# Optimization experiments

Measured on AMD Instinct MI355X. Metric: run time of the kernel, lower is better.

Reference implementation:

```python
import jax, jax.numpy as jnp
import numpy as np

N_NODES = 50000
N_EDGES = 600000
D_OBJ = 128
D_REL = 128
D_OUT = 128


def setup_inputs() -> dict:
    key = jax.random.key(0)
    ks = jax.random.split(key, 7)
    s_obj = 1.0 / np.sqrt(D_OBJ)
    s_rel = 1.0 / np.sqrt(D_REL)
    return {
        "obj_vecs": jax.random.normal(ks[0], (N_NODES, D_OBJ), dtype=jnp.float32),
        "rel_vecs": jax.random.normal(ks[1], (N_EDGES, D_REL), dtype=jnp.float32),
        "edge_index": jax.random.randint(ks[2], (N_EDGES, 2), 0, N_NODES, dtype=jnp.int64),
        "W_obj": jax.random.normal(ks[3], (D_OUT, D_OBJ), dtype=jnp.float32) * s_obj,
        "b_obj": jax.random.normal(ks[4], (D_OUT,), dtype=jnp.float32) * s_obj,
        "W_rel": jax.random.normal(ks[5], (D_OUT, D_REL), dtype=jnp.float32) * s_rel,
        "b_rel": jax.random.normal(ks[6], (D_OUT,), dtype=jnp.float32) * s_rel,
    }


def reference(obj_vecs, rel_vecs, edge_index, W_obj, b_obj, W_rel, b_rel):
    # Per-node linear once ([N, d_out]) instead of twice per edge -- same math
    # since lin_obj(x_i) + lin_obj(x_j) = (x_i W^T + b) + (x_j W^T + b).
    obj_lin = obj_vecs @ W_obj.T + b_obj            # [N, d_out]
    rel_lin = rel_vecs @ W_rel.T + b_rel            # [E, d_out]
    src = edge_index[:, 0]
    dst = edge_index[:, 1]
    # message = relu(lin_obj(obj_i) + lin_rel(rel_k) + lin_obj(obj_j))
    msg = jax.nn.relu(obj_lin[src] + rel_lin + obj_lin[dst])  # [E, d_out]
    # aggr='add', flow source_to_target: scatter-add at target nodes (col 1)
    aggr = jax.ops.segment_sum(msg, dst, num_segments=obj_vecs.shape[0])
    return jax.nn.relu(aggr)
```

## Files before the change

kernel.cpp:

```cpp
#include <hip/hip_runtime.h>

#define N_NODES 50000
#define N_EDGES 600000
#define DD 128

typedef __attribute__((ext_vector_type(8))) short short8;
typedef __attribute__((ext_vector_type(4))) float f32x4;

__device__ __forceinline__ short f2bf(float f) {
    union { float f; unsigned u; } v; v.f = f;
    unsigned r = v.u + 0x7fffu + ((v.u >> 16) & 1u);
    return (short)(r >> 16);
}
__device__ __forceinline__ float bf2f(short s) {
    union { float f; unsigned u; } v; v.u = ((unsigned)(unsigned short)s) << 16;
    return v.f;
}
__device__ __forceinline__ float u2f(unsigned u) {
    union { float f; unsigned u; } v; v.u = u;
    return v.f;
}
__device__ __forceinline__ unsigned packbf(float a, float b) {
    return ((unsigned)(unsigned short)f2bf(a)) |
           (((unsigned)(unsigned short)f2bf(b)) << 16);
}

__global__ __launch_bounds__(256) void k_lin(const float* __restrict__ X,
                                             const float* __restrict__ W,
                                             const float* __restrict__ bias,
                                             short* __restrict__ Y,
                                             int ntiles) {
    __shared__ __align__(16) short Wf[128 * 128];
    for (int i = threadIdx.x; i < 2048; i += 256) {
        const int fl = i & 63, fr = i >> 6;
        const int nt = fr >> 2, ks = fr & 3, fg = fl >> 4, fln = fl & 15;
        const float* s = W + (nt * 16 + fln) * DD + ks * 32 + fg * 8;
        short* d = Wf + i * 8;
#pragma unroll
        for (int j = 0; j < 8; ++j) d[j] = f2bf(s[j]);
    }
    __syncthreads();

    const int wave = threadIdx.x >> 6;
    const int lane = threadIdx.x & 63;
    const int g = lane >> 4, ln = lane & 15;

    float bb[8];
#pragma unroll
    for (int nt = 0; nt < 8; ++nt) bb[nt] = bias[nt * 16 + ln];

    for (int t = blockIdx.x * 4 + wave; t < ntiles; t += gridDim.x * 4) {
        const float* xr = X + (size_t)(t * 16 + ln) * DD;
        short8 a[4];
#pragma unroll
        for (int ks = 0; ks < 4; ++ks) {
            const f32x4* p = (const f32x4*)(xr + ks * 32 + g * 8);
            const f32x4 t0 = __builtin_nontemporal_load(p);
            const f32x4 t1 = __builtin_nontemporal_load(p + 1);
            short8 v;
            v[0] = f2bf(t0[0]); v[1] = f2bf(t0[1]); v[2] = f2bf(t0[2]); v[3] = f2bf(t0[3]);
            v[4] = f2bf(t1[0]); v[5] = f2bf(t1[1]); v[6] = f2bf(t1[2]); v[7] = f2bf(t1[3]);
            a[ks] = v;
        }
#pragma unroll
        for (int nt = 0; nt < 8; ++nt) {
            f32x4 acc = {0.f, 0.f, 0.f, 0.f};
#pragma unroll
            for (int ks = 0; ks < 4; ++ks) {
                short8 b = *(const short8*)(Wf + (((nt << 2) + ks) * 64 + lane) * 8);
                acc = __builtin_amdgcn_mfma_f32_16x16x32_bf16(a[ks], b, acc, 0, 0, 0);
            }
#pragma unroll
            for (int r = 0; r < 4; ++r)
                Y[(size_t)(t * 16 + g * 4 + r) * DD + nt * 16 + ln] = f2bf(acc[r] + bb[nt]);
        }
    }
}

__global__ __launch_bounds__(256) void k_count(const int* __restrict__ EI,
                                               int* __restrict__ counts) {
    int e = blockIdx.x * 256 + threadIdx.x;
    if (e < N_EDGES) atomicAdd(&counts[EI[2 * e + 1]], 1);
}

__global__ __launch_bounds__(256) void k_scan1(const int* __restrict__ counts,
                                               int* __restrict__ scanned,
                                               int* __restrict__ bsum) {
    __shared__ int tmp[256];
    const int t = threadIdx.x;
    const int i = blockIdx.x * 256 + t;
    int v = (i < N_NODES) ? counts[i] : 0;
    tmp[t] = v;
    __syncthreads();
#pragma unroll
    for (int off = 1; off < 256; off <<= 1) {
        int x = (t >= off) ? tmp[t - off] : 0;
        __syncthreads();
        tmp[t] += x;
        __syncthreads();
    }
    if (i < N_NODES) scanned[i] = tmp[t] - v;
    if (t == 255) bsum[blockIdx.x] = tmp[255];
}

__global__ __launch_bounds__(256) void k_scan3m(const int* __restrict__ scanned,
                                                const int* __restrict__ bsum,
                                                int* __restrict__ offsets,
                                                int* __restrict__ cursor,
                                                int nb) {
    __shared__ int red[256];
    const int t = threadIdx.x;
    const int bid = blockIdx.x;
    red[t] = (t < bid && t < nb) ? bsum[t] : 0;
    __syncthreads();
#pragma unroll
    for (int off = 128; off > 0; off >>= 1) {
        if (t < off) red[t] += red[t + off];
        __syncthreads();
    }
    const int pre = red[0];
    const int i = bid * 256 + t;
    if (i < N_NODES) {
        const int off = scanned[i] + pre;
        offsets[i] = off;
        cursor[i] = off;
    }
    if (i == 0) offsets[N_NODES] = N_EDGES;
}

__global__ __launch_bounds__(256) void k_scatter2(const int* __restrict__ EI,
                                                  int* __restrict__ cursor,
                                                  int* __restrict__ perm) {
    int e = blockIdx.x * 256 + threadIdx.x;
    if (e < N_EDGES)
        perm[e] = atomicAdd(&cursor[EI[2 * e + 1]], 1);
}

__global__ __launch_bounds__(256) void k_fl(const float* __restrict__ RV,
                                            const int* __restrict__ EI,
                                            const int* __restrict__ perm,
                                            const float* __restrict__ W,
                                            const float* __restrict__ bias,
                                            const short* __restrict__ OL,
                                            unsigned* __restrict__ Ysw) {
    __shared__ __align__(16) short Wf[128 * 128];
    __shared__ __align__(16) unsigned stg[4][8 * 136];

    for (int i = threadIdx.x; i < 2048; i += 256) {
        const int fl = i & 63, fr = i >> 6;
        const int nt = fr >> 2, ks = fr & 3, fg = fl >> 4, fln = fl & 15;
        const float* s = W + (nt * 16 + fln) * DD + ks * 32 + fg * 8;
        short* d = Wf + i * 8;
#pragma unroll
        for (int j = 0; j < 8; ++j) d[j] = f2bf(s[j]);
    }
    __syncthreads();

    const int wave = threadIdx.x >> 6;
    const int lane = threadIdx.x & 63;
    const int g = lane >> 4, ln = lane & 15;
    unsigned* st = stg[wave];

    const float br0 = bias[2 * lane];
    const float br1 = bias[2 * lane + 1];
    const unsigned short* OLu = (const unsigned short*)OL;
    const int NT = N_EDGES / 16;

    for (int t = blockIdx.x * 4 + wave; t < NT; t += gridDim.x * 4) {
        const int e0 = t * 16;

        const float* xr = RV + (size_t)(e0 + ln) * DD;
        short8 a[4];
#pragma unroll
        for (int ks = 0; ks < 4; ++ks) {
            const f32x4* p = (const f32x4*)(xr + ks * 32 + g * 8);
            const f32x4 t0 = __builtin_nontemporal_load(p);
            const f32x4 t1 = __builtin_nontemporal_load(p + 1);
            short8 v;
            v[0] = f2bf(t0[0]); v[1] = f2bf(t0[1]); v[2] = f2bf(t0[2]); v[3] = f2bf(t0[3]);
            v[4] = f2bf(t1[0]); v[5] = f2bf(t1[1]); v[6] = f2bf(t1[2]); v[7] = f2bf(t1[3]);
            a[ks] = v;
        }

        int sp = 0, pp = 0;
        if (lane < 16) {
            sp = EI[2 * (e0 + lane)];
            pp = perm[e0 + lane];
        }

        f32x4 acc[8];
#pragma unroll
        for (int nt = 0; nt < 8; ++nt) {
            acc[nt] = (f32x4){0.f, 0.f, 0.f, 0.f};
#pragma unroll
            for (int ks = 0; ks < 4; ++ks) {
                short8 b = *(const short8*)(Wf + (((nt << 2) + ks) * 64 + lane) * 8);
                acc[nt] = __builtin_amdgcn_mfma_f32_16x16x32_bf16(a[ks], b, acc[nt], 0, 0, 0);
            }
        }

#pragma unroll
        for (int nt = 0; nt < 8; ++nt) {
            const int c = nt * 16 + ln;
            st[(g * 2) * 136 + c]     = packbf(acc[nt][0], acc[nt][1]);
            st[(g * 2 + 1) * 136 + c] = packbf(acc[nt][2], acc[nt][3]);
        }

#pragma unroll
        for (int ep = 0; ep < 8; ++ep) {
            const unsigned qx = st[ep * 136 + 2 * lane];
            const unsigned qy = st[ep * 136 + 2 * lane + 1];
#pragma unroll
            for (int sub = 0; sub < 2; ++sub) {
                const int e = 2 * ep + sub;
                const int src = __shfl(sp, e);
                const int pos = __shfl(pp, e);
                const float s0 = sub ? u2f(qx & 0xffff0000u) : u2f(qx << 16);
                const float s1 = sub ? u2f(qy & 0xffff0000u) : u2f(qy << 16);
                const unsigned olw = *(const unsigned*)(OLu + (size_t)src * DD + 2 * lane);
                const float y0 = s0 + br0 + u2f(olw << 16);
                const float y1 = s1 + br1 + u2f(olw & 0xffff0000u);
                Ysw[(size_t)pos * (DD / 2) + lane] = packbf(y0, y1);
            }
        }
    }
}

__global__ __launch_bounds__(256) void k_segsum(const unsigned* __restrict__ Ysw,
                                                const short* __restrict__ OL,
                                                const int* __restrict__ offs,
                                                float* __restrict__ out) {
    const int wave = threadIdx.x >> 6;
    const int lane = threadIdx.x & 63;
    const int v = blockIdx.x * 4 + wave;
    if (v >= N_NODES) return;

    const int r0 = offs[v], r1 = offs[v + 1];
    const int half = lane >> 5;
    const int q = lane & 31;
    const unsigned short* OLu = (const unsigned short*)OL;

    const uint2 odw = *(const uint2*)(OLu + (size_t)v * DD + 4 * q);
    const float od0 = u2f(odw.x << 16), od1 = u2f(odw.x & 0xffff0000u);
    const float od2 = u2f(odw.y << 16), od3 = u2f(odw.y & 0xffff0000u);

    float a0 = 0.f, a1 = 0.f, a2 = 0.f, a3 = 0.f;
    for (int r = r0 + half; r < r1; r += 2) {
        const uint2 y = *(const uint2*)(Ysw + (size_t)r * (DD / 2) + 2 * q);
        a0 += fmaxf(u2f(y.x << 16) + od0, 0.f);
        a1 += fmaxf(u2f(y.x & 0xffff0000u) + od1, 0.f);
        a2 += fmaxf(u2f(y.y << 16) + od2, 0.f);
        a3 += fmaxf(u2f(y.y & 0xffff0000u) + od3, 0.f);
    }
    a0 += __shfl_xor(a0, 32);
    a1 += __shfl_xor(a1, 32);
    a2 += __shfl_xor(a2, 32);
    a3 += __shfl_xor(a3, 32);

    if (half == 0) {
        float4 o;
        o.x = fmaxf(a0, 0.f); o.y = fmaxf(a1, 0.f);
        o.z = fmaxf(a2, 0.f); o.w = fmaxf(a3, 0.f);
        *(float4*)(out + (size_t)v * DD + 4 * q) = o;
    }
}

extern "C" void kernel_launch(void* const* d_in, const int* in_sizes, int n_in,
                              void* d_out, int out_size, void* d_ws, size_t ws_size,
                              hipStream_t stream) {
    const float* obj = (const float*)d_in[0];
    const float* rel = (const float*)d_in[1];
    const int*   ei  = (const int*)d_in[2];
    const float* Wo  = (const float*)d_in[3];
    const float* bo  = (const float*)d_in[4];
    const float* Wr  = (const float*)d_in[5];
    const float* br  = (const float*)d_in[6];
    float* out = (float*)d_out;

    char* ws = (char*)d_ws;
    unsigned* Ysw  = (unsigned*)ws;
    short* OLb     = (short*)(ws + 153600000);
    int*   perm    = (int*)(ws + 166400000);
    int*   counts  = (int*)(ws + 168800000);
    int*   scanned = (int*)(ws + 169000192);
    int*   offsets = (int*)(ws + 169200896);
    int*   cursor  = (int*)(ws + 169401600);
    int*   bsum    = (int*)(ws + 169601792);

    const int NB_E = (N_EDGES + 255) / 256;
    const int NB_N = (N_NODES + 255) / 256;

    hipMemsetAsync(counts, 0, N_NODES * sizeof(int), stream);
    k_count<<<NB_E, 256, 0, stream>>>(ei, counts);
    k_scan1<<<NB_N, 256, 0, stream>>>(counts, scanned, bsum);
    k_scan3m<<<NB_N, 256, 0, stream>>>(scanned, bsum, offsets, cursor, NB_N);
    k_scatter2<<<NB_E, 256, 0, stream>>>(ei, cursor, perm);
    k_lin<<<782, 256, 0, stream>>>(obj, Wo, bo, OLb, N_NODES / 16);
    k_fl<<<2048, 256, 0, stream>>>(rel, ei, perm, Wr, br, OLb, Ysw);
    k_segsum<<<(N_NODES + 3) / 4, 256, 0, stream>>>(Ysw, OLb, offsets, out);
}
```

Baseline: 238.2 us.

## Fuse edge linear with segmented aggregation over destination-sorted edges

Instead of writing a bf16 per-edge message buffer in permuted order and reducing it in a separate segment-sum kernel, edges are sorted by destination (storing edge id and source) and each wave processes a fixed run of 80 sorted edges. It gathers rel rows, runs the MFMA linear, and accumulates relu messages directly into the output, using atomics only for segments shared across run boundaries. This removes the large intermediate buffer write and read, at the cost of gathered (non-contiguous) rel_vecs loads, an extra zero-fill and relu pass, and float atomics. The second gather of obj_lin[dst] per edge is now done inside the fused kernel.

```diff
diff --git a/kernel.cpp b/kernel.cpp
--- a/kernel.cpp
+++ b/kernel.cpp
@@ -3,6 +3,8 @@
 #define N_NODES 50000
 #define N_EDGES 600000
 #define DD 128
+#define RUNE 80
+#define NBLK_AGG 1875
 
 typedef __attribute__((ext_vector_type(8))) short short8;
 typedef __attribute__((ext_vector_type(4))) float f32x4;
@@ -11,10 +13,6 @@
     union { float f; unsigned u; } v; v.f = f;
     unsigned r = v.u + 0x7fffu + ((v.u >> 16) & 1u);
     return (short)(r >> 16);
-}
-__device__ __forceinline__ float bf2f(short s) {
-    union { float f; unsigned u; } v; v.u = ((unsigned)(unsigned short)s) << 16;
-    return v.f;
 }
 __device__ __forceinline__ float u2f(unsigned u) {
     union { float f; unsigned u; } v; v.u = u;
@@ -54,9 +52,8 @@
         short8 a[4];
 #pragma unroll
         for (int ks = 0; ks < 4; ++ks) {
-            const f32x4* p = (const f32x4*)(xr + ks * 32 + g * 8);
-            const f32x4 t0 = __builtin_nontemporal_load(p);
-            const f32x4 t1 = __builtin_nontemporal_load(p + 1);
+            const f32x4 t0 = *(const f32x4*)(xr + ks * 32 + g * 8);
+            const f32x4 t1 = *(const f32x4*)(xr + ks * 32 + g * 8 + 4);
             short8 v;
             v[0] = f2bf(t0[0]); v[1] = f2bf(t0[1]); v[2] = f2bf(t0[2]); v[3] = f2bf(t0[3]);
             v[4] = f2bf(t1[0]); v[5] = f2bf(t1[1]); v[6] = f2bf(t1[2]); v[7] = f2bf(t1[3]);
@@ -105,7 +102,6 @@
 
 __global__ __launch_bounds__(256) void k_scan3m(const int* __restrict__ scanned,
                                                 const int* __restrict__ bsum,
-                                                int* __restrict__ offsets,
                                                 int* __restrict__ cursor,
                                                 int nb) {
     __shared__ int red[256];
@@ -120,29 +116,29 @@
     }
     const int pre = red[0];
     const int i = bid * 256 + t;
-    if (i < N_NODES) {
-        const int off = scanned[i] + pre;
-        offsets[i] = off;
-        cursor[i] = off;
-    }
-    if (i == 0) offsets[N_NODES] = N_EDGES;
-}
-
-__global__ __launch_bounds__(256) void k_scatter2(const int* __restrict__ EI,
+    if (i < N_NODES) cursor[i] = scanned[i] + pre;
+}
+
+__global__ __launch_bounds__(256) void k_scatter3(const int* __restrict__ EI,
                                                   int* __restrict__ cursor,
-                                                  int* __restrict__ perm) {
+                                                  int2* __restrict__ sorted,
+                                                  int* __restrict__ dsts) {
     int e = blockIdx.x * 256 + threadIdx.x;
-    if (e < N_EDGES)
-        perm[e] = atomicAdd(&cursor[EI[2 * e + 1]], 1);
-}
-
-__global__ __launch_bounds__(256) void k_fl(const float* __restrict__ RV,
-                                            const int* __restrict__ EI,
-                                            const int* __restrict__ perm,
-                                            const float* __restrict__ W,
-                                            const float* __restrict__ bias,
-                                            const short* __restrict__ OL,
-                                            unsigned* __restrict__ Ysw) {
+    if (e < N_EDGES) {
+        int2 sd = *(const int2*)(EI + 2 * e);
+        int pos = atomicAdd(&cursor[sd.y], 1);
+        sorted[pos] = make_int2(e, sd.x);
+        dsts[pos] = sd.y;
+    }
+}
+
+__global__ __launch_bounds__(256) void k_fagg2(const float* __restrict__ RV,
+                                               const int2* __restrict__ sorted,
+                                               const int* __restrict__ dsts,
+                                               const float* __restrict__ W,
+                                               const float* __restrict__ bias,
+                                               const short* __restrict__ OL,
+                                               float* __restrict__ out) {
     __shared__ __align__(16) short Wf[128 * 128];
     __shared__ __align__(16) unsigned stg[4][8 * 136];
 
@@ -161,33 +157,58 @@
     const int g = lane >> 4, ln = lane & 15;
     unsigned* st = stg[wave];
 
+    const int wid = blockIdx.x * 4 + wave;
+    const int p0 = wid * RUNE;
+    const int p1 = p0 + RUNE;
+
     const float br0 = bias[2 * lane];
     const float br1 = bias[2 * lane + 1];
     const unsigned short* OLu = (const unsigned short*)OL;
-    const int NT = N_EDGES / 16;
-
-    for (int t = blockIdx.x * 4 + wave; t < NT; t += gridDim.x * 4) {
-        const int e0 = t * 16;
-
-        const float* xr = RV + (size_t)(e0 + ln) * DD;
-        short8 a[4];
+
+    const bool head_shared = (p0 > 0) && (dsts[p0 - 1] == dsts[p0]);
+    const bool tail_shared = (p1 < N_EDGES) && (dsts[p1] == dsts[p1 - 1]);
+
+    int d_cur = dsts[p0];
+    bool head_atomic = head_shared;
+    float a0 = 0.f, a1 = 0.f;
+
+    int2 se_c = sorted[p0 + ln];
+    int  dl_c = dsts[p0 + ln];
+    f32x4 ar_c[8];
+    {
+        const float* base = RV + (size_t)se_c.x * DD;
 #pragma unroll
         for (int ks = 0; ks < 4; ++ks) {
-            const f32x4* p = (const f32x4*)(xr + ks * 32 + g * 8);
-            const f32x4 t0 = __builtin_nontemporal_load(p);
-            const f32x4 t1 = __builtin_nontemporal_load(p + 1);
+            ar_c[2 * ks]     = *(const f32x4*)(base + ks * 32 + g * 8);
+            ar_c[2 * ks + 1] = *(const f32x4*)(base + ks * 32 + g * 8 + 4);
+        }
+    }
+
+    for (int k = 0; k < RUNE / 16; ++k) {
+        int2 se_n = se_c; int dl_n = dl_c;
+        f32x4 ar_n[8];
+        const bool have = (k + 1) < (RUNE / 16);
+        if (have) {
+            const int e0n = p0 + (k + 1) * 16;
+            se_n = sorted[e0n + ln];
+            dl_n = dsts[e0n + ln];
+            const float* base = RV + (size_t)se_n.x * DD;
+#pragma unroll
+            for (int ks = 0; ks < 4; ++ks) {
+                ar_n[2 * ks]     = *(const f32x4*)(base + ks * 32 + g * 8);
+                ar_n[2 * ks + 1] = *(const f32x4*)(base + ks * 32 + g * 8 + 4);
+            }
+        }
+
+        short8 af[4];
+#pragma unroll
+        for (int ks = 0; ks < 4; ++ks) {
+            const f32x4 t0 = ar_c[2 * ks], t1 = ar_c[2 * ks + 1];
             short8 v;
             v[0] = f2bf(t0[0]); v[1] = f2bf(t0[1]); v[2] = f2bf(t0[2]); v[3] = f2bf(t0[3]);
             v[4] = f2bf(t1[0]); v[5] = f2bf(t1[1]); v[6] = f2bf(t1[2]); v[7] = f2bf(t1[3]);
-            a[ks] = v;
-        }
-
-        int sp = 0, pp = 0;
-        if (lane < 16) {
-            sp = EI[2 * (e0 + lane)];
-            pp = perm[e0 + lane];
-        }
-
+            af[ks] = v;
+        }
         f32x4 acc[8];
 #pragma unroll
         for (int nt = 0; nt < 8; ++nt) {
@@ -195,7 +216,7 @@
 #pragma unroll
             for (int ks = 0; ks < 4; ++ks) {
                 short8 b = *(const short8*)(Wf + (((nt << 2) + ks) * 64 + lane) * 8);
-                acc[nt] = __builtin_amdgcn_mfma_f32_16x16x32_bf16(a[ks], b, acc[nt], 0, 0, 0);
+                acc[nt] = __builtin_amdgcn_mfma_f32_16x16x32_bf16(af[ks], b, acc[nt], 0, 0, 0);
             }
         }
 
@@ -213,55 +234,58 @@
 #pragma unroll
             for (int sub = 0; sub < 2; ++sub) {
                 const int e = 2 * ep + sub;
-                const int src = __shfl(sp, e);
-                const int pos = __shfl(pp, e);
+                const int src  = __shfl(se_c.y, e);
+                const int dstv = __shfl(dl_c, e);
+                if (dstv != d_cur) {
+                    if (head_atomic) {
+                        atomicAdd(&out[(size_t)d_cur * DD + 2 * lane], a0);
+                        atomicAdd(&out[(size_t)d_cur * DD + 2 * lane + 1], a1);
+                        head_atomic = false;
+                    } else {
+                        *(float2*)(out + (size_t)d_cur * DD + 2 * lane) =
+                            make_float2(a0, a1);
+                    }
+                    a0 = a1 = 0.f;
+                    d_cur = dstv;
+                }
                 const float s0 = sub ? u2f(qx & 0xffff0000u) : u2f(qx << 16);
                 const float s1 = sub ? u2f(qy & 0xffff0000u) : u2f(qy << 16);
-                const unsigned olw = *(const unsigned*)(OLu + (size_t)src * DD + 2 * lane);
-                const float y0 = s0 + br0 + u2f(olw << 16);
-                const float y1 = s1 + br1 + u2f(olw & 0xffff0000u);
-                Ysw[(size_t)pos * (DD / 2) + lane] = packbf(y0, y1);
+                const unsigned ows = *(const unsigned*)(OLu + (size_t)src  * DD + 2 * lane);
+                const unsigned owd = *(const unsigned*)(OLu + (size_t)dstv * DD + 2 * lane);
+                const float m0 = s0 + br0 + u2f(ows << 16) + u2f(owd << 16);
+                const float m1 = s1 + br1 + u2f(ows & 0xffff0000u) + u2f(owd & 0xffff0000u);
+                a0 += fmaxf(m0, 0.f);
+                a1 += fmaxf(m1, 0.f);
             }
         }
-    }
-}
-
-__global__ __launch_bounds__(256) void k_segsum(const unsigned* __restrict__ Ysw,
-                                                const short* __restrict__ OL,
-                                                const int* __restrict__ offs,
-                                                float* __restrict__ out) {
-    const int wave = threadIdx.x >> 6;
-    const int lane = threadIdx.x & 63;
-    const int v = blockIdx.x * 4 + wave;
-    if (v >= N_NODES) return;
-
-    const int r0 = offs[v], r1 = offs[v + 1];
-    const int half = lane >> 5;
-    const int q = lane & 31;
-    const unsigned short* OLu = (const unsigned short*)OL;
-
-    const uint2 odw = *(const uint2*)(OLu + (size_t)v * DD + 4 * q);
-    const float od0 = u2f(odw.x << 16), od1 = u2f(odw.x & 0xffff0000u);
-    const float od2 = u2f(odw.y << 16), od3 = u2f(odw.y & 0xffff0000u);
-
-    float a0 = 0.f, a1 = 0.f, a2 = 0.f, a3 = 0.f;
-    for (int r = r0 + half; r < r1; r += 2) {
-        const uint2 y = *(const uint2*)(Ysw + (size_t)r * (DD / 2) + 2 * q);
-        a0 += fmaxf(u2f(y.x << 16) + od0, 0.f);
-        a1 += fmaxf(u2f(y.x & 0xffff0000u) + od1, 0.f);
-        a2 += fmaxf(u2f(y.y << 16) + od2, 0.f);
-        a3 += fmaxf(u2f(y.y & 0xffff0000u) + od3, 0.f);
-    }
-    a0 += __shfl_xor(a0, 32);
-    a1 += __shfl_xor(a1, 32);
-    a2 += __shfl_xor(a2, 32);
-    a3 += __shfl_xor(a3, 32);
-
-    if (half == 0) {
-        float4 o;
-        o.x = fmaxf(a0, 0.f); o.y = fmaxf(a1, 0.f);
-        o.z = fmaxf(a2, 0.f); o.w = fmaxf(a3, 0.f);
-        *(float4*)(out + (size_t)v * DD + 4 * q) = o;
+
+        if (have) {
+            se_c = se_n; dl_c = dl_n;
+#pragma unroll
+            for (int q = 0; q < 8; ++q) ar_c[q] = ar_n[q];
+        }
+    }
+
+    if (head_atomic || tail_shared) {
+        atomicAdd(&out[(size_t)d_cur * DD + 2 * lane], a0);
+        atomicAdd(&out[(size_t)d_cur * DD + 2 * lane + 1], a1);
+    } else {
+        *(float2*)(out + (size_t)d_cur * DD + 2 * lane) = make_float2(a0, a1);
+    }
+}
+
+__global__ __launch_bounds__(256) void k_zerof(float4* __restrict__ p, int n4) {
+    int i = blockIdx.x * 256 + threadIdx.x;
+    if (i < n4) p[i] = (float4){0.f, 0.f, 0.f, 0.f};
+}
+
+__global__ __launch_bounds__(256) void k_relu(float4* __restrict__ p, int n4) {
+    int i = blockIdx.x * 256 + threadIdx.x;
+    if (i < n4) {
+        float4 v = p[i];
+        v.x = fmaxf(v.x, 0.f); v.y = fmaxf(v.y, 0.f);
+        v.z = fmaxf(v.z, 0.f); v.w = fmaxf(v.w, 0.f);
+        p[i] = v;
     }
 }
 
@@ -278,24 +302,25 @@
     float* out = (float*)d_out;
 
     char* ws = (char*)d_ws;
-    unsigned* Ysw  = (unsigned*)ws;
-    short* OLb     = (short*)(ws + 153600000);
-    int*   perm    = (int*)(ws + 166400000);
-    int*   counts  = (int*)(ws + 168800000);
-    int*   scanned = (int*)(ws + 169000192);
-    int*   offsets = (int*)(ws + 169200896);
-    int*   cursor  = (int*)(ws + 169401600);
-    int*   bsum    = (int*)(ws + 169601792);
+    short* OLb     = (short*)ws;
+    int2*  sorted  = (int2*)(ws + 12800000);
+    int*   dsts    = (int*)(ws + 17600000);
+    int*   counts  = (int*)(ws + 20000000);
+    int*   scanned = (int*)(ws + 20200192);
+    int*   cursor  = (int*)(ws + 20400896);
+    int*   bsum    = (int*)(ws + 20601088);
 
     const int NB_E = (N_EDGES + 255) / 256;
     const int NB_N = (N_NODES + 255) / 256;
+    const int n4 = N_NODES * DD / 4;
 
     hipMemsetAsync(counts, 0, N_NODES * sizeof(int), stream);
     k_count<<<NB_E, 256, 0, stream>>>(ei, counts);
     k_scan1<<<NB_N, 256, 0, stream>>>(counts, scanned, bsum);
-    k_scan3m<<<NB_N, 256, 0, stream>>>(scanned, bsum, offsets, cursor, NB_N);
-    k_scatter2<<<NB_E, 256, 0, stream>>>(ei, cursor, perm);
+    k_scan3m<<<NB_N, 256, 0, stream>>>(scanned, bsum, cursor, NB_N);
+    k_scatter3<<<NB_E, 256, 0, stream>>>(ei, cursor, sorted, dsts);
     k_lin<<<782, 256, 0, stream>>>(obj, Wo, bo, OLb, N_NODES / 16);
-    k_fl<<<2048, 256, 0, stream>>>(rel, ei, perm, Wr, br, OLb, Ysw);
-    k_segsum<<<(N_NODES + 3) / 4, 256, 0, stream>>>(Ysw, OLb, offsets, out);
-}
+    k_zerof<<<(n4 + 255) / 256, 256, 0, stream>>>((float4*)out, n4);
+    k_fagg2<<<NBLK_AGG, 256, 0, stream>>>(rel, sorted, dsts, Wr, br, OLb, out);
+    k_relu<<<(n4 + 255) / 256, 256, 0, stream>>>((float4*)out, n4);
+}
```

After: 413.2 us. 1.73x slower.
